# Kernel optimization log

Measured on AMD Instinct MI355X. Metric: run time of the kernel, lower is better.

Reference implementation:

```python
import jax, jax.numpy as jnp
import numpy as np

DIM = 384
HEADS = 6
HEAD_DIM = DIM // HEADS
HIDDEN = int(DIM * 4.0)
LS_INIT = 1e-5
EPS = 1e-5


def _ln(x, w, b):
    mu = jnp.mean(x, axis=-1, keepdims=True)
    var = jnp.var(x, axis=-1, keepdims=True)
    return (x - mu) * jax.lax.rsqrt(var + EPS) * w + b


def setup_inputs() -> dict:
    key = jax.random.key(0)
    ks = jax.random.split(key, 12)
    s = 0.02
    eye = jnp.eye(HIDDEN, dtype=jnp.float32)
    return {
        "x": jax.random.normal(ks[0], (8, 2048, DIM), dtype=jnp.float32),
        "qkv_w": jax.random.normal(ks[1], (3 * DIM, DIM), dtype=jnp.float32) * s,
        "qkv_b": jnp.zeros((3 * DIM,), dtype=jnp.float32),
        "proj_w": jax.random.normal(ks[2], (DIM, DIM), dtype=jnp.float32) * s,
        "proj_b": jnp.zeros((DIM,), dtype=jnp.float32),
        "fc1_w": jax.random.normal(ks[3], (HIDDEN, DIM), dtype=jnp.float32) * s,
        "fc1_b": jnp.zeros((HIDDEN,), dtype=jnp.float32),
        "eye1_w": eye + jax.random.normal(ks[4], (HIDDEN, HIDDEN), dtype=jnp.float32) * s,
        "eye2_w": eye + jax.random.normal(ks[5], (HIDDEN, HIDDEN), dtype=jnp.float32) * s,
        "fc2_w": jax.random.normal(ks[6], (DIM, HIDDEN), dtype=jnp.float32) * s,
        "fc2_b": jnp.zeros((DIM,), dtype=jnp.float32),
        "norm1_w": jnp.ones((DIM,), dtype=jnp.float32),
        "norm1_b": jnp.zeros((DIM,), dtype=jnp.float32),
        "norm2_w": jnp.ones((DIM,), dtype=jnp.float32),
        "norm2_b": jnp.zeros((DIM,), dtype=jnp.float32),
        "ls1_gamma": jnp.full((DIM,), LS_INIT, dtype=jnp.float32),
        "ls2_gamma": jnp.full((DIM,), LS_INIT, dtype=jnp.float32),
    }


def reference(x, qkv_w, qkv_b, proj_w, proj_b, fc1_w, fc1_b, eye1_w, eye2_w,
              fc2_w, fc2_b, norm1_w, norm1_b, norm2_w, norm2_b, ls1_gamma, ls2_gamma):
    B, N, C = x.shape
    scale = HEAD_DIM ** -0.5

    # ---- attention branch ----
    h = _ln(x, norm1_w, norm1_b)
    qkv = h @ qkv_w.T + qkv_b                      # [B,N,3C]
    qkv = qkv.reshape(B, N, 3, HEADS, HEAD_DIM)
    q = qkv[:, :, 0].transpose(0, 2, 1, 3) * scale  # [B,H,N,D]
    k = qkv[:, :, 1].transpose(0, 2, 1, 3)
    v = qkv[:, :, 2].transpose(0, 2, 1, 3)
    attn = jax.nn.softmax(jnp.einsum('bhnd,bhmd->bhnm', q, k), axis=-1)  # [B,H,N,N]
    o = jnp.einsum('bhnm,bhmd->bhnd', attn, v)
    o = o.transpose(0, 2, 1, 3).reshape(B, N, C)
    o = o @ proj_w.T + proj_b
    x = x + o * ls1_gamma

    # ---- extended MLP branch (timm Mlp norm is Identity) ----
    h2 = _ln(x, norm2_w, norm2_b)
    a = jax.nn.gelu(h2 @ fc1_w.T + fc1_b, approximate=False)
    a = (a @ eye1_w.T) @ eye2_w.T
    a = a @ fc2_w.T + fc2_b
    return x + a * ls2_gamma
```

## Files before the change

kernel.cpp:

```cpp
#include <hip/hip_runtime.h>
#include <math.h>

#define DIM 384
#define HEADS 6
#define HEAD_DIM 64
#define HIDDEN 1536
#define BATCH 8
#define SEQ 2048
#define TOKENS (BATCH * SEQ)

typedef __bf16 bf16;
typedef float f32x4 __attribute__((ext_vector_type(4)));
typedef float f32x16 __attribute__((ext_vector_type(16)));
typedef int i32x2 __attribute__((ext_vector_type(2)));
typedef int i32x4 __attribute__((ext_vector_type(4)));
typedef int i32x8 __attribute__((ext_vector_type(8)));

#define GLOAD_LDS(gp, lp)                                                      \
    __builtin_amdgcn_global_load_lds(                                          \
        (const __attribute__((address_space(1))) void*)(gp),                   \
        (__attribute__((address_space(3))) void*)(lp), 16, 0, 0)

__device__ __forceinline__ unsigned char to_fp8(float v) {
    return (unsigned char)(__builtin_amdgcn_cvt_pk_fp8_f32(v, v, 0, false) & 0xff);
}

__device__ __forceinline__ i32x8 pack8(i32x4 lo, i32x4 hi) {
    i32x8 r;
#pragma unroll
    for (int j = 0; j < 4; j++) { r[j] = lo[j]; r[4 + j] = hi[j]; }
    return r;
}

#define NW_QKV  (1152 * 384)
#define NW_PROJ (384 * 384)
#define NW_FC1  (1536 * 384)
#define NW_EYE  (1536 * 1536)
#define NW_FC2  (384 * 1536)
#define NW_ALL2 (NW_QKV + NW_PROJ + NW_FC1 + NW_EYE + NW_FC2)

__global__ void convert_w8(const float* __restrict__ qkv, const float* __restrict__ proj,
                           const float* __restrict__ fc1, const float* __restrict__ e2,
                           const float* __restrict__ fc2, unsigned char* __restrict__ dst) {
    int q4 = blockIdx.x * 256 + threadIdx.x;
    int stride = gridDim.x * 256;
    for (; q4 < NW_ALL2 / 4; q4 += stride) {
        int i = q4 * 4;
        int j = i;
        const float* src;
        if (j < NW_QKV) src = qkv;
        else if ((j -= NW_QKV) < NW_PROJ) src = proj;
        else if ((j -= NW_PROJ) < NW_FC1) src = fc1;
        else if ((j -= NW_FC1) < NW_EYE) src = e2;
        else { j -= NW_EYE; src = fc2; }
        float4 v = *(const float4*)(src + j);
        int p = __builtin_amdgcn_cvt_pk_fp8_f32(v.x, v.y, 0, false);
        p = __builtin_amdgcn_cvt_pk_fp8_f32(v.z, v.w, p, true);
        *(int*)(dst + i) = p;
    }
}

__global__ __launch_bounds__(256) void transpose_f8(const float* __restrict__ in,
                                                    unsigned char* __restrict__ outT) {
    __shared__ float t[64][65];
    int r0 = blockIdx.y * 64, c0 = blockIdx.x * 64;
    int tc = threadIdx.x & 63, tr = threadIdx.x >> 6;
#pragma unroll
    for (int i = 0; i < 16; i++) {
        int r = tr + 4 * i;
        t[r][tc] = in[(size_t)(r0 + r) * 1536 + c0 + tc];
    }
    __syncthreads();
    int on = threadIdx.x >> 2;
    int ok0 = (threadIdx.x & 3) * 16;
    i32x4 pk;
#pragma unroll
    for (int q = 0; q < 4; q++) {
        int p = __builtin_amdgcn_cvt_pk_fp8_f32(t[ok0 + 4 * q + 0][on],
                                                t[ok0 + 4 * q + 1][on], 0, false);
        p = __builtin_amdgcn_cvt_pk_fp8_f32(t[ok0 + 4 * q + 2][on],
                                            t[ok0 + 4 * q + 3][on], p, true);
        pk[q] = p;
    }
    *(i32x4*)(outT + (size_t)(c0 + on) * 1536 + r0 + ok0) = pk;
}

__global__ __launch_bounds__(256) void ln_kernel(const float* __restrict__ x,
                                                 const float* __restrict__ w,
                                                 const float* __restrict__ b,
                                                 unsigned char* __restrict__ out) {
    int wave = threadIdx.x >> 6;
    int lane = threadIdx.x & 63;
    int t = blockIdx.x * 4 + wave;
    const float* xr = x + (size_t)t * DIM;
    float v[6];
    float s = 0.f;
#pragma unroll
    for (int i = 0; i < 6; i++) { v[i] = xr[lane + 64 * i]; s += v[i]; }
#pragma unroll
    for (int m = 1; m < 64; m <<= 1) s += __shfl_xor(s, m, 64);
    float mu = s * (1.f / DIM);
    float q = 0.f;
#pragma unroll
    for (int i = 0; i < 6; i++) { float d = v[i] - mu; q += d * d; }
#pragma unroll
    for (int m = 1; m < 64; m <<= 1) q += __shfl_xor(q, m, 64);
    float rstd = rsqrtf(q * (1.f / DIM) + 1e-5f);
    unsigned char* orow = out + (size_t)t * DIM;
#pragma unroll
    for (int i = 0; i < 6; i++) {
        int c = lane + 64 * i;
        orow[c] = to_fp8((v[i] - mu) * rstd * w[c] + b[c]);
    }
}

template <int EPI>
__global__ __launch_bounds__(256) void gemm_f8(const unsigned char* __restrict__ A,
                                               const unsigned char* __restrict__ W,
                                               const float* __restrict__ bias,
                                               float* __restrict__ outf,
                                               const float* __restrict__ resid,
                                               const float* __restrict__ gamma,
                                               unsigned char* __restrict__ vtb8,
                                               unsigned char* __restrict__ out8,
                                               int N, int K) {
    __shared__ __attribute__((aligned(16))) unsigned char As[128 * 128];
    __shared__ __attribute__((aligned(16))) unsigned char Bs[128 * 128];
    int tid = threadIdx.x;
    int wave = tid >> 6, lane = tid & 63;
    int l15 = lane & 15, quad = lane >> 4;
    int bm = blockIdx.y * 128, bn = blockIdx.x * 128;
    int wm = (wave & 1) * 64, wn = (wave >> 1) * 64;
    f32x4 acc[4][4] = {};

    for (int k0 = 0; k0 < K; k0 += 128) {
#pragma unroll
        for (int i = 0; i < 4; i++) {
            int slot = i * 256 + tid;
            int rr = slot >> 3;
            int gg = (slot & 7) ^ (rr & 7);
            GLOAD_LDS(A + (size_t)(bm + rr) * K + k0 + gg * 16,
                      (char*)As + (i * 256 + wave * 64) * 16);
            GLOAD_LDS(W + (size_t)(bn + rr) * K + k0 + gg * 16,
                      (char*)Bs + (i * 256 + wave * 64) * 16);
        }
        __syncthreads();
        i32x8 af[4], bfr[4];
#pragma unroll
        for (int mt = 0; mt < 4; mt++) {
            int rA = wm + mt * 16 + l15;
            const i32x4* p = (const i32x4*)(As + 128 * rA);
            af[mt] = pack8(p[(2 * quad) ^ (rA & 7)], p[(2 * quad + 1) ^ (rA & 7)]);
        }
#pragma unroll
        for (int nt = 0; nt < 4; nt++) {
            int rB = wn + nt * 16 + l15;
            const i32x4* p = (const i32x4*)(Bs + 128 * rB);
            bfr[nt] = pack8(p[(2 * quad) ^ (rB & 7)], p[(2 * quad + 1) ^ (rB & 7)]);
        }
#pragma unroll
        for (int mt = 0; mt < 4; mt++)
#pragma unroll
            for (int nt = 0; nt < 4; nt++)
                acc[mt][nt] = __builtin_amdgcn_mfma_scale_f32_16x16x128_f8f6f4(
                    af[mt], bfr[nt], acc[mt][nt], 0, 0,
                    0, 0x7f7f7f7f, 0, 0x7f7f7f7f);
        __syncthreads();
    }

#pragma unroll
    for (int mt = 0; mt < 4; mt++) {
#pragma unroll
        for (int nt = 0; nt < 4; nt++) {
            int col = bn + wn + nt * 16 + l15;
            int row0 = bm + wm + mt * 16 + quad * 4;
            float v[4];
#pragma unroll
            for (int r = 0; r < 4; r++) {
                v[r] = acc[mt][nt][r];
                if (EPI >= 2) v[r] += bias[col];
                if (EPI == 2) v[r] = 0.5f * v[r] * (1.f + erff(v[r] * 0.70710678118654752f));
            }
            if (EPI == 3) {
#pragma unroll
                for (int r = 0; r < 4; r++) {
                    size_t idx = (size_t)(row0 + r) * N + col;
                    outf[idx] = resid[idx] + v[r] * gamma[col];
                }
            } else if (EPI == 4) {
                if (col < 768) {
                    float sc = (col < 384) ? 0.180336880f : 1.f;
#pragma unroll
                    for (int r = 0; r < 4; r++)
                        out8[(size_t)(row0 + r) * 768 + col] = to_fp8(v[r] * sc);
                } else {
                    int hd = col - 768;
                    int b = row0 >> 11;
                    int n0 = row0 & 2047;
                    int p = __builtin_amdgcn_cvt_pk_fp8_f32(v[0], v[1], 0, false);
                    p = __builtin_amdgcn_cvt_pk_fp8_f32(v[2], v[3], p, true);
                    *(int*)(vtb8 + ((size_t)(b * 384 + hd) << 11) + n0) = p;
                }
            } else {
#pragma unroll
                for (int r = 0; r < 4; r++)
                    out8[(size_t)(row0 + r) * N + col] = to_fp8(v[r]);
            }
        }
    }
}

__global__ __launch_bounds__(256, 3) void attn_kernel(const unsigned char* __restrict__ qk8,
                                                      const unsigned char* __restrict__ vtb8,
                                                      unsigned char* __restrict__ o) {
    __shared__ __attribute__((aligned(16))) unsigned char Ks[2][64 * 64];
    __shared__ __attribute__((aligned(16))) unsigned char Vts[2][64 * 64];
    int tid = threadIdx.x, wave = tid >> 6, lane = tid & 63;
    int l31 = lane & 31, h = lane >> 5;
    int bh = blockIdx.y;
    int b = bh / HEADS, hh = bh - b * HEADS;
    int qr0 = blockIdx.x * 128 + wave * 32;
    const unsigned char* base = qk8 + (size_t)b * SEQ * 768;
    const unsigned char* vbase = vtb8 + ((size_t)bh << 17);

    int rr = tid >> 2, ss = tid & 3;
    int fs = (rr >> 1) & 3;
    const unsigned char* kg = base + (size_t)rr * 768 + 384 + hh * 64 + 16 * (ss ^ fs);
    const unsigned char* vg = vbase + ((size_t)rr << 11) + 16 * (ss ^ fs);
    int ldsoff = tid * 16;

    i32x8 aq = *(const i32x8*)(base + (size_t)(qr0 + l31) * 768 + hh * 64 + 32 * h);

    f32x16 oa0 = {}, oa1 = {};
    float lsum = 0.f;
    int swr = (l31 >> 1) & 3;

    GLOAD_LDS(kg, (char*)Ks[0] + ldsoff);
    GLOAD_LDS(vg, (char*)Vts[0] + ldsoff);
    __syncthreads();

    for (int kt = 0; kt < SEQ / 64; kt++) {
        const unsigned char* Kc = Ks[kt & 1];
        const unsigned char* Vc = Vts[kt & 1];
        if (kt + 1 < SEQ / 64) {
            GLOAD_LDS(kg + (size_t)(kt + 1) * 64 * 768, (char*)Ks[(kt + 1) & 1] + ldsoff);
            GLOAD_LDS(vg + (kt + 1) * 64, (char*)Vts[(kt + 1) & 1] + ldsoff);
        }

        int pk[2][4];
#pragma unroll
        for (int mi = 0; mi < 2; mi++) {
            int rK = 32 * mi + l31;
            const i32x4* kp = (const i32x4*)(Kc + rK * 64);
            i32x8 ak = pack8(kp[(2 * h + 0) ^ swr], kp[(2 * h + 1) ^ swr]);
            f32x16 s = {};
            s = __builtin_amdgcn_mfma_scale_f32_32x32x64_f8f6f4(
                ak, aq, s, 0, 0, 0, 0x7f7f7f7f, 0, 0x7f7f7f7f);
#pragma unroll
            for (int g = 0; g < 4; g++) {
                float p0 = __builtin_amdgcn_exp2f(s[4 * g + 0]);
                float p1 = __builtin_amdgcn_exp2f(s[4 * g + 1]);
                float p2 = __builtin_amdgcn_exp2f(s[4 * g + 2]);
                float p3 = __builtin_amdgcn_exp2f(s[4 * g + 3]);
                lsum += (p0 + p1) + (p2 + p3);
                int pkv = __builtin_amdgcn_cvt_pk_fp8_f32(p0, p1, 0, false);
                pkv = __builtin_amdgcn_cvt_pk_fp8_f32(p2, p3, pkv, true);
                pk[mi][g] = pkv;
            }
        }

        i32x8 ap;
#pragma unroll
        for (int g = 0; g < 4; g++) {
            i32x2 r = __builtin_amdgcn_permlane32_swap(pk[0][g], pk[1][g], false, false);
            ap[2 * g] = r[0];
            ap[2 * g + 1] = r[1];
        }

        {
            const i32x4* vp0 = (const i32x4*)(Vc + l31 * 64);
            i32x8 bv0 = pack8(vp0[(2 * h + 0) ^ swr], vp0[(2 * h + 1) ^ swr]);
            oa0 = __builtin_amdgcn_mfma_scale_f32_32x32x64_f8f6f4(
                ap, bv0, oa0, 0, 0, 0, 0x7f7f7f7f, 0, 0x7f7f7f7f);
            const i32x4* vp1 = (const i32x4*)(Vc + (32 + l31) * 64);
            i32x8 bv1 = pack8(vp1[(2 * h + 0) ^ swr], vp1[(2 * h + 1) ^ swr]);
            oa1 = __builtin_amdgcn_mfma_scale_f32_32x32x64_f8f6f4(
                ap, bv1, oa1, 0, 0, 0, 0x7f7f7f7f, 0, 0x7f7f7f7f);
        }
        __syncthreads();
    }

    lsum += __shfl_xor(lsum, 32, 64);

#pragma unroll
    for (int g = 0; g < 4; g++) {
#pragma unroll
        for (int r4 = 0; r4 < 4; r4++) {
            int qloc = r4 + 8 * g + 4 * h;
            float inv = 1.f / __shfl(lsum, qloc, 64);
            int r = 4 * g + r4;
            unsigned char* orow = o + ((size_t)(b * SEQ + qr0 + qloc)) * DIM + hh * 64;
            orow[l31]      = to_fp8(oa0[r] * inv);
            orow[32 + l31] = to_fp8(oa1[r] * inv);
        }
    }
}

extern "C" void kernel_launch(void* const* d_in, const int* in_sizes, int n_in,
                              void* d_out, int out_size, void* d_ws, size_t ws_size,
                              hipStream_t stream) {
    const float* x      = (const float*)d_in[0];
    const float* qkv_w  = (const float*)d_in[1];
    const float* qkv_b  = (const float*)d_in[2];
    const float* proj_w = (const float*)d_in[3];
    const float* proj_b = (const float*)d_in[4];
    const float* fc1_w  = (const float*)d_in[5];
    const float* fc1_b  = (const float*)d_in[6];
    const float* eye1_w = (const float*)d_in[7];
    const float* eye2_w = (const float*)d_in[8];
    const float* fc2_w  = (const float*)d_in[9];
    const float* fc2_b  = (const float*)d_in[10];
    const float* n1w    = (const float*)d_in[11];
    const float* n1b    = (const float*)d_in[12];
    const float* n2w    = (const float*)d_in[13];
    const float* n2b    = (const float*)d_in[14];
    const float* ls1    = (const float*)d_in[15];
    const float* ls2    = (const float*)d_in[16];
    float* out = (float*)d_out;

    char* w = (char*)d_ws;
    size_t off = 0;
    unsigned char* w8 = (unsigned char*)(w + off); off += (size_t)NW_ALL2;
    unsigned char* wqkv8  = w8;
    unsigned char* wproj8 = wqkv8 + NW_QKV;
    unsigned char* wfc18  = wproj8 + NW_PROJ;
    unsigned char* weye28 = wfc18 + NW_FC1;
    unsigned char* wfc28  = weye28 + NW_EYE;
    unsigned char* e1t8  = (unsigned char*)(w + off); off += (size_t)NW_EYE;
    unsigned char* m1t8  = (unsigned char*)(w + off); off += (size_t)NW_EYE;
    unsigned char* wc8   = (unsigned char*)(w + off); off += (size_t)NW_FC2;
    unsigned char* hbuf8 = (unsigned char*)(w + off); off += (size_t)TOKENS * DIM;
    unsigned char* qk8   = (unsigned char*)(w + off); off += (size_t)TOKENS * 768;
    unsigned char* vtb8  = (unsigned char*)(w + off); off += (size_t)TOKENS * DIM;
    unsigned char* obuf8 = (unsigned char*)(w + off); off += (size_t)TOKENS * DIM;
    unsigned char* abuf8 = (unsigned char*)(w + off); off += (size_t)TOKENS * HIDDEN;
    float* x1   = (float*)(w + off); off += (size_t)TOKENS * DIM * 4;

    convert_w8<<<4096, 256, 0, stream>>>(qkv_w, proj_w, fc1_w, eye2_w, fc2_w, w8);

    transpose_f8<<<dim3(24, 24), 256, 0, stream>>>(eye1_w, e1t8);

    gemm_f8<0><<<dim3(1536 / 128, 1536 / 128), 256, 0, stream>>>(
        e1t8, weye28, nullptr, nullptr, nullptr, nullptr, nullptr, m1t8, 1536, 1536);

    gemm_f8<0><<<dim3(1536 / 128, 384 / 128), 256, 0, stream>>>(
        wfc28, m1t8, nullptr, nullptr, nullptr, nullptr, nullptr, wc8, 1536, 1536);

    ln_kernel<<<TOKENS / 4, 256, 0, stream>>>(x, n1w, n1b, hbuf8);

    gemm_f8<4><<<dim3(1152 / 128, TOKENS / 128), 256, 0, stream>>>(
        hbuf8, wqkv8, qkv_b, nullptr, nullptr, nullptr, vtb8, qk8, 1152, 384);

    attn_kernel<<<dim3(SEQ / 128, BATCH * HEADS), 256, 0, stream>>>(qk8, vtb8, obuf8);

    gemm_f8<3><<<dim3(384 / 128, TOKENS / 128), 256, 0, stream>>>(
        obuf8, wproj8, proj_b, x1, x, ls1, nullptr, nullptr, 384, 384);

    ln_kernel<<<TOKENS / 4, 256, 0, stream>>>(x1, n2w, n2b, hbuf8);

    gemm_f8<2><<<dim3(1536 / 128, TOKENS / 128), 256, 0, stream>>>(
        hbuf8, wfc18, fc1_b, nullptr, nullptr, nullptr, nullptr, abuf8, 1536, 384);

    gemm_f8<3><<<dim3(384 / 128, TOKENS / 128), 256, 0, stream>>>(
        abuf8, wc8, fc2_b, out, x1, ls2, nullptr, nullptr, 384, 1536);
}
```

Before: 294.9 us.

## Process 64 query rows per wave in attention to reuse K/V fragments

The attention kernel now runs 2 waves per block, and each wave handles 64 query rows as two 32-row halves instead of 32 rows. Each K and V fragment read from LDS feeds two MFMAs instead of one, halving LDS fragment reads per unit of work, and each thread issues two async global-to-LDS loads per tile instead of one. In exchange there are fewer waves per block, more accumulator registers per wave, and lower occupancy, which may reduce latency hiding.

```diff
diff --git a/kernel.cpp b/kernel.cpp
--- a/kernel.cpp
+++ b/kernel.cpp
@@ -210,98 +210,130 @@
     }
 }
 
-__global__ __launch_bounds__(256, 3) void attn_kernel(const unsigned char* __restrict__ qk8,
+__global__ __launch_bounds__(128, 2) void attn_kernel(const unsigned char* __restrict__ qk8,
                                                       const unsigned char* __restrict__ vtb8,
                                                       unsigned char* __restrict__ o) {
     __shared__ __attribute__((aligned(16))) unsigned char Ks[2][64 * 64];
     __shared__ __attribute__((aligned(16))) unsigned char Vts[2][64 * 64];
-    int tid = threadIdx.x, wave = tid >> 6, lane = tid & 63;
+    int tid = threadIdx.x, lane = tid & 63;
+    int wave = tid >> 6;
     int l31 = lane & 31, h = lane >> 5;
     int bh = blockIdx.y;
     int b = bh / HEADS, hh = bh - b * HEADS;
-    int qr0 = blockIdx.x * 128 + wave * 32;
+    int qw0 = blockIdx.x * 128 + wave * 64;
     const unsigned char* base = qk8 + (size_t)b * SEQ * 768;
     const unsigned char* vbase = vtb8 + ((size_t)bh << 17);
 
-    int rr = tid >> 2, ss = tid & 3;
-    int fs = (rr >> 1) & 3;
-    const unsigned char* kg = base + (size_t)rr * 768 + 384 + hh * 64 + 16 * (ss ^ fs);
-    const unsigned char* vg = vbase + ((size_t)rr << 11) + 16 * (ss ^ fs);
-    int ldsoff = tid * 16;
-
-    i32x8 aq = *(const i32x8*)(base + (size_t)(qr0 + l31) * 768 + hh * 64 + 32 * h);
-
-    f32x16 oa0 = {}, oa1 = {};
-    float lsum = 0.f;
+    int c0 = tid, c1 = tid + 128;
+    int rr0 = c0 >> 2, ss0 = c0 & 3, fs0 = (rr0 >> 1) & 3;
+    int rr1 = c1 >> 2, ss1 = c1 & 3, fs1 = (rr1 >> 1) & 3;
+    const unsigned char* kg0 = base + (size_t)rr0 * 768 + 384 + hh * 64 + 16 * (ss0 ^ fs0);
+    const unsigned char* kg1 = base + (size_t)rr1 * 768 + 384 + hh * 64 + 16 * (ss1 ^ fs1);
+    const unsigned char* vg0 = vbase + ((size_t)rr0 << 11) + 16 * (ss0 ^ fs0);
+    const unsigned char* vg1 = vbase + ((size_t)rr1 << 11) + 16 * (ss1 ^ fs1);
+    int lo0 = c0 * 16, lo1 = c1 * 16;
+
+    i32x8 aq0 = *(const i32x8*)(base + (size_t)(qw0 + l31) * 768 + hh * 64 + 32 * h);
+    i32x8 aq1 = *(const i32x8*)(base + (size_t)(qw0 + 32 + l31) * 768 + hh * 64 + 32 * h);
+
+    f32x16 oa00 = {}, oa01 = {}, oa10 = {}, oa11 = {};
+    float ls0 = 0.f, ls1v = 0.f;
     int swr = (l31 >> 1) & 3;
 
-    GLOAD_LDS(kg, (char*)Ks[0] + ldsoff);
-    GLOAD_LDS(vg, (char*)Vts[0] + ldsoff);
+    GLOAD_LDS(kg0, (char*)Ks[0] + lo0);
+    GLOAD_LDS(kg1, (char*)Ks[0] + lo1);
+    GLOAD_LDS(vg0, (char*)Vts[0] + lo0);
+    GLOAD_LDS(vg1, (char*)Vts[0] + lo1);
     __syncthreads();
 
     for (int kt = 0; kt < SEQ / 64; kt++) {
         const unsigned char* Kc = Ks[kt & 1];
         const unsigned char* Vc = Vts[kt & 1];
         if (kt + 1 < SEQ / 64) {
-            GLOAD_LDS(kg + (size_t)(kt + 1) * 64 * 768, (char*)Ks[(kt + 1) & 1] + ldsoff);
-            GLOAD_LDS(vg + (kt + 1) * 64, (char*)Vts[(kt + 1) & 1] + ldsoff);
-        }
-
-        int pk[2][4];
+            char* kn = (char*)Ks[(kt + 1) & 1];
+            char* vn = (char*)Vts[(kt + 1) & 1];
+            GLOAD_LDS(kg0 + (size_t)(kt + 1) * 64 * 768, kn + lo0);
+            GLOAD_LDS(kg1 + (size_t)(kt + 1) * 64 * 768, kn + lo1);
+            GLOAD_LDS(vg0 + (kt + 1) * 64, vn + lo0);
+            GLOAD_LDS(vg1 + (kt + 1) * 64, vn + lo1);
+        }
+
+        int pk[2][2][4];
 #pragma unroll
         for (int mi = 0; mi < 2; mi++) {
             int rK = 32 * mi + l31;
             const i32x4* kp = (const i32x4*)(Kc + rK * 64);
             i32x8 ak = pack8(kp[(2 * h + 0) ^ swr], kp[(2 * h + 1) ^ swr]);
-            f32x16 s = {};
-            s = __builtin_amdgcn_mfma_scale_f32_32x32x64_f8f6f4(
-                ak, aq, s, 0, 0, 0, 0x7f7f7f7f, 0, 0x7f7f7f7f);
-#pragma unroll
-            for (int g = 0; g < 4; g++) {
-                float p0 = __builtin_amdgcn_exp2f(s[4 * g + 0]);
-                float p1 = __builtin_amdgcn_exp2f(s[4 * g + 1]);
-                float p2 = __builtin_amdgcn_exp2f(s[4 * g + 2]);
-                float p3 = __builtin_amdgcn_exp2f(s[4 * g + 3]);
-                lsum += (p0 + p1) + (p2 + p3);
-                int pkv = __builtin_amdgcn_cvt_pk_fp8_f32(p0, p1, 0, false);
-                pkv = __builtin_amdgcn_cvt_pk_fp8_f32(p2, p3, pkv, true);
-                pk[mi][g] = pkv;
+#pragma unroll
+            for (int qh = 0; qh < 2; qh++) {
+                f32x16 s = {};
+                s = __builtin_amdgcn_mfma_scale_f32_32x32x64_f8f6f4(
+                    ak, (qh ? aq1 : aq0), s, 0, 0, 0, 0x7f7f7f7f, 0, 0x7f7f7f7f);
+                float lsum = 0.f;
+#pragma unroll
+                for (int g = 0; g < 4; g++) {
+                    float p0 = __builtin_amdgcn_exp2f(s[4 * g + 0]);
+                    float p1 = __builtin_amdgcn_exp2f(s[4 * g + 1]);
+                    float p2 = __builtin_amdgcn_exp2f(s[4 * g + 2]);
+                    float p3 = __builtin_amdgcn_exp2f(s[4 * g + 3]);
+                    lsum += (p0 + p1) + (p2 + p3);
+                    int pkv = __builtin_amdgcn_cvt_pk_fp8_f32(p0, p1, 0, false);
+                    pkv = __builtin_amdgcn_cvt_pk_fp8_f32(p2, p3, pkv, true);
+                    pk[qh][mi][g] = pkv;
+                }
+                if (qh) ls1v += lsum; else ls0 += lsum;
             }
         }
 
-        i32x8 ap;
+        i32x8 ap0, ap1;
 #pragma unroll
         for (int g = 0; g < 4; g++) {
-            i32x2 r = __builtin_amdgcn_permlane32_swap(pk[0][g], pk[1][g], false, false);
-            ap[2 * g] = r[0];
-            ap[2 * g + 1] = r[1];
+            i32x2 r0 = __builtin_amdgcn_permlane32_swap(pk[0][0][g], pk[0][1][g], false, false);
+            ap0[2 * g] = r0[0];
+            ap0[2 * g + 1] = r0[1];
+            i32x2 r1 = __builtin_amdgcn_permlane32_swap(pk[1][0][g], pk[1][1][g], false, false);
+            ap1[2 * g] = r1[0];
+            ap1[2 * g + 1] = r1[1];
         }
 
         {
             const i32x4* vp0 = (const i32x4*)(Vc + l31 * 64);
             i32x8 bv0 = pack8(vp0[(2 * h + 0) ^ swr], vp0[(2 * h + 1) ^ swr]);
-            oa0 = __builtin_amdgcn_mfma_scale_f32_32x32x64_f8f6f4(
-                ap, bv0, oa0, 0, 0, 0, 0x7f7f7f7f, 0, 0x7f7f7f7f);
+            oa00 = __builtin_amdgcn_mfma_scale_f32_32x32x64_f8f6f4(
+                ap0, bv0, oa00, 0, 0, 0, 0x7f7f7f7f, 0, 0x7f7f7f7f);
+            oa10 = __builtin_amdgcn_mfma_scale_f32_32x32x64_f8f6f4(
+                ap1, bv0, oa10, 0, 0, 0, 0x7f7f7f7f, 0, 0x7f7f7f7f);
             const i32x4* vp1 = (const i32x4*)(Vc + (32 + l31) * 64);
             i32x8 bv1 = pack8(vp1[(2 * h + 0) ^ swr], vp1[(2 * h + 1) ^ swr]);
-            oa1 = __builtin_amdgcn_mfma_scale_f32_32x32x64_f8f6f4(
-                ap, bv1, oa1, 0, 0, 0, 0x7f7f7f7f, 0, 0x7f7f7f7f);
+            oa01 = __builtin_amdgcn_mfma_scale_f32_32x32x64_f8f6f4(
+                ap0, bv1, oa01, 0, 0, 0, 0x7f7f7f7f, 0, 0x7f7f7f7f);
+            oa11 = __builtin_amdgcn_mfma_scale_f32_32x32x64_f8f6f4(
+                ap1, bv1, oa11, 0, 0, 0, 0x7f7f7f7f, 0, 0x7f7f7f7f);
         }
         __syncthreads();
     }
 
-    lsum += __shfl_xor(lsum, 32, 64);
+    ls0 += __shfl_xor(ls0, 32, 64);
+    ls1v += __shfl_xor(ls1v, 32, 64);
 
 #pragma unroll
     for (int g = 0; g < 4; g++) {
 #pragma unroll
         for (int r4 = 0; r4 < 4; r4++) {
             int qloc = r4 + 8 * g + 4 * h;
-            float inv = 1.f / __shfl(lsum, qloc, 64);
             int r = 4 * g + r4;
-            unsigned char* orow = o + ((size_t)(b * SEQ + qr0 + qloc)) * DIM + hh * 64;
-            orow[l31]      = to_fp8(oa0[r] * inv);
-            orow[32 + l31] = to_fp8(oa1[r] * inv);
+            {
+                float inv = 1.f / __shfl(ls0, qloc, 64);
+                unsigned char* orow = o + ((size_t)(b * SEQ + qw0 + qloc)) * DIM + hh * 64;
+                orow[l31]      = to_fp8(oa00[r] * inv);
+                orow[32 + l31] = to_fp8(oa01[r] * inv);
+            }
+            {
+                float inv = 1.f / __shfl(ls1v, qloc, 64);
+                unsigned char* orow = o + ((size_t)(b * SEQ + qw0 + 32 + qloc)) * DIM + hh * 64;
+                orow[l31]      = to_fp8(oa10[r] * inv);
+                orow[32 + l31] = to_fp8(oa11[r] * inv);
+            }
         }
     }
 }
@@ -361,7 +393,7 @@
     gemm_f8<4><<<dim3(1152 / 128, TOKENS / 128), 256, 0, stream>>>(
         hbuf8, wqkv8, qkv_b, nullptr, nullptr, nullptr, vtb8, qk8, 1152, 384);
 
-    attn_kernel<<<dim3(SEQ / 128, BATCH * HEADS), 256, 0, stream>>>(qk8, vtb8, obuf8);
+    attn_kernel<<<dim3(SEQ / 128, BATCH * HEADS), 128, 0, stream>>>(qk8, vtb8, obuf8);
 
     gemm_f8<3><<<dim3(384 / 128, TOKENS / 128), 256, 0, stream>>>(
         obuf8, wproj8, proj_b, x1, x, ls1, nullptr, nullptr, 384, 384);
```

New measurement: 304.5 us. 3.3% more time.

## Double-buffer LDS tiles in fp8 GEMM to overlap global loads with MFMA

Applied to the files above, without the earlier changes.

Doubles the shared-memory A/B tiles and prefetches the next K-tile with global_load_lds while the current tile feeds the MFMAs. This hides global-memory latency behind compute. It doubles LDS use to 64KB per block, which may lower occupancy. Correctness depends on the single barrier per iteration also covering completion of the async LDS loads.

```diff
diff --git a/kernel.cpp b/kernel.cpp
--- a/kernel.cpp
+++ b/kernel.cpp
@@ -124,8 +124,8 @@
                                                unsigned char* __restrict__ vtb8,
                                                unsigned char* __restrict__ out8,
                                                int N, int K) {
-    __shared__ __attribute__((aligned(16))) unsigned char As[128 * 128];
-    __shared__ __attribute__((aligned(16))) unsigned char Bs[128 * 128];
+    __shared__ __attribute__((aligned(16))) unsigned char As[2][128 * 128];
+    __shared__ __attribute__((aligned(16))) unsigned char Bs[2][128 * 128];
     int tid = threadIdx.x;
     int wave = tid >> 6, lane = tid & 63;
     int l15 = lane & 15, quad = lane >> 4;
@@ -133,29 +133,40 @@
     int wm = (wave & 1) * 64, wn = (wave >> 1) * 64;
     f32x4 acc[4][4] = {};
 
-    for (int k0 = 0; k0 < K; k0 += 128) {
-#pragma unroll
-        for (int i = 0; i < 4; i++) {
-            int slot = i * 256 + tid;
-            int rr = slot >> 3;
-            int gg = (slot & 7) ^ (rr & 7);
-            GLOAD_LDS(A + (size_t)(bm + rr) * K + k0 + gg * 16,
-                      (char*)As + (i * 256 + wave * 64) * 16);
-            GLOAD_LDS(W + (size_t)(bn + rr) * K + k0 + gg * 16,
-                      (char*)Bs + (i * 256 + wave * 64) * 16);
-        }
-        __syncthreads();
+    int nk = K >> 7;
+    int ldst = (tid & 192) * 16;
+#define STAGE_TILE(buf, kbase)                                                  \
+    do {                                                                        \
+        _Pragma("unroll")                                                       \
+        for (int i = 0; i < 4; i++) {                                           \
+            int slot = i * 256 + tid;                                           \
+            int rr = slot >> 3;                                                 \
+            int gg = (slot & 7) ^ (rr & 7);                                     \
+            GLOAD_LDS(A + (size_t)(bm + rr) * K + (kbase) + gg * 16,            \
+                      (char*)As[buf] + i * 4096 + ldst);                        \
+            GLOAD_LDS(W + (size_t)(bn + rr) * K + (kbase) + gg * 16,            \
+                      (char*)Bs[buf] + i * 4096 + ldst);                        \
+        }                                                                       \
+    } while (0)
+
+    STAGE_TILE(0, 0);
+    __syncthreads();
+
+    for (int kt = 0; kt < nk; kt++) {
+        int cur = kt & 1;
+        if (kt + 1 < nk) STAGE_TILE(cur ^ 1, (kt + 1) << 7);
+
         i32x8 af[4], bfr[4];
 #pragma unroll
         for (int mt = 0; mt < 4; mt++) {
             int rA = wm + mt * 16 + l15;
-            const i32x4* p = (const i32x4*)(As + 128 * rA);
+            const i32x4* p = (const i32x4*)(As[cur] + 128 * rA);
             af[mt] = pack8(p[(2 * quad) ^ (rA & 7)], p[(2 * quad + 1) ^ (rA & 7)]);
         }
 #pragma unroll
         for (int nt = 0; nt < 4; nt++) {
             int rB = wn + nt * 16 + l15;
-            const i32x4* p = (const i32x4*)(Bs + 128 * rB);
+            const i32x4* p = (const i32x4*)(Bs[cur] + 128 * rB);
             bfr[nt] = pack8(p[(2 * quad) ^ (rB & 7)], p[(2 * quad + 1) ^ (rB & 7)]);
         }
 #pragma unroll
@@ -167,6 +178,7 @@
                     0, 0x7f7f7f7f, 0, 0x7f7f7f7f);
         __syncthreads();
     }
+#undef STAGE_TILE
 
 #pragma unroll
     for (int mt = 0; mt < 4; mt++) {
```

Result: no change. 298.0 us (+1.0%).

## Fuse proj GEMM with residual and LayerNorm2; raise MFMA priority in attention

Applied to the files above, without the earlier changes.

Adds a new full-row GEMM kernel for the output projection. Each block computes 64 tokens across all 384 columns, applies bias, layer-scale and residual, writes x1, then runs LayerNorm2 in registers and writes the fp8 input for fc1. This removes the separate ln_kernel launch and its re-read of x1, at the cost of a large LDS footprint (56KB) and 96 accumulator registers per thread, which may limit occupancy. The attention kernel also wraps its MFMAs in s_setprio and hoists the second V fragment load ahead of the PV MFMAs.

```diff
diff --git a/kernel.cpp b/kernel.cpp
--- a/kernel.cpp
+++ b/kernel.cpp
@@ -210,6 +210,91 @@
     }
 }
 
+__global__ __launch_bounds__(256) void gemm_proj_ln(const unsigned char* __restrict__ A,
+                                                    const unsigned char* __restrict__ W,
+                                                    const float* __restrict__ bias,
+                                                    const float* __restrict__ resid,
+                                                    const float* __restrict__ gamma,
+                                                    const float* __restrict__ n2w,
+                                                    const float* __restrict__ n2b,
+                                                    float* __restrict__ x1,
+                                                    unsigned char* __restrict__ hbuf8) {
+    __shared__ __attribute__((aligned(16))) unsigned char As[64 * 128];
+    __shared__ __attribute__((aligned(16))) unsigned char Bs[384 * 128];
+    int tid = threadIdx.x;
+    int wave = tid >> 6, lane = tid & 63;
+    int l15 = lane & 15, quad = lane >> 4;
+    int bm = blockIdx.x * 64;
+    int wm = wave * 16;
+    f32x4 acc[24];
+#pragma unroll
+    for (int i = 0; i < 24; i++) acc[i] = (f32x4){0.f, 0.f, 0.f, 0.f};
+
+    const int K = 384;
+    for (int k0 = 0; k0 < K; k0 += 128) {
+#pragma unroll
+        for (int i = 0; i < 2; i++) {
+            int slot = i * 256 + tid;
+            int rr = slot >> 3, gg = (slot & 7) ^ (rr & 7);
+            GLOAD_LDS(A + (size_t)(bm + rr) * K + k0 + gg * 16, (char*)As + slot * 16);
+        }
+#pragma unroll
+        for (int i = 0; i < 12; i++) {
+            int slot = i * 256 + tid;
+            int rr = slot >> 3, gg = (slot & 7) ^ (rr & 7);
+            GLOAD_LDS(W + (size_t)rr * K + k0 + gg * 16, (char*)Bs + slot * 16);
+        }
+        __syncthreads();
+        int rA = wm + l15;
+        const i32x4* pa = (const i32x4*)(As + 128 * rA);
+        i32x8 af = pack8(pa[(2 * quad) ^ (rA & 7)], pa[(2 * quad + 1) ^ (rA & 7)]);
+#pragma unroll
+        for (int nt = 0; nt < 24; nt++) {
+            int rB = nt * 16 + l15;
+            const i32x4* pb = (const i32x4*)(Bs + 128 * rB);
+            i32x8 bf = pack8(pb[(2 * quad) ^ (rB & 7)], pb[(2 * quad + 1) ^ (rB & 7)]);
+            acc[nt] = __builtin_amdgcn_mfma_scale_f32_16x16x128_f8f6f4(
+                af, bf, acc[nt], 0, 0, 0, 0x7f7f7f7f, 0, 0x7f7f7f7f);
+        }
+        __syncthreads();
+    }
+
+    int row0 = bm + wm + quad * 4;
+#pragma unroll
+    for (int nt = 0; nt < 24; nt++) {
+        int col = nt * 16 + l15;
+        float bi = bias[col], ga = gamma[col];
+#pragma unroll
+        for (int r = 0; r < 4; r++) {
+            size_t idx = (size_t)(row0 + r) * DIM + col;
+            float v = resid[idx] + (acc[nt][r] + bi) * ga;
+            x1[idx] = v;
+            acc[nt][r] = v;
+        }
+    }
+#pragma unroll
+    for (int r = 0; r < 4; r++) {
+        float s = 0.f;
+#pragma unroll
+        for (int nt = 0; nt < 24; nt++) s += acc[nt][r];
+#pragma unroll
+        for (int m = 1; m < 16; m <<= 1) s += __shfl_xor(s, m, 64);
+        float mu = s * (1.f / DIM);
+        float q = 0.f;
+#pragma unroll
+        for (int nt = 0; nt < 24; nt++) { float d = acc[nt][r] - mu; q += d * d; }
+#pragma unroll
+        for (int m = 1; m < 16; m <<= 1) q += __shfl_xor(q, m, 64);
+        float rstd = rsqrtf(q * (1.f / DIM) + 1e-5f);
+        unsigned char* orow = hbuf8 + (size_t)(row0 + r) * DIM;
+#pragma unroll
+        for (int nt = 0; nt < 24; nt++) {
+            int col = nt * 16 + l15;
+            orow[col] = to_fp8((acc[nt][r] - mu) * rstd * n2w[col] + n2b[col]);
+        }
+    }
+}
+
 __global__ __launch_bounds__(256, 3) void attn_kernel(const unsigned char* __restrict__ qk8,
                                                       const unsigned char* __restrict__ vtb8,
                                                       unsigned char* __restrict__ o) {
@@ -254,8 +339,10 @@
             const i32x4* kp = (const i32x4*)(Kc + rK * 64);
             i32x8 ak = pack8(kp[(2 * h + 0) ^ swr], kp[(2 * h + 1) ^ swr]);
             f32x16 s = {};
+            __builtin_amdgcn_s_setprio(1);
             s = __builtin_amdgcn_mfma_scale_f32_32x32x64_f8f6f4(
                 ak, aq, s, 0, 0, 0, 0x7f7f7f7f, 0, 0x7f7f7f7f);
+            __builtin_amdgcn_s_setprio(0);
 #pragma unroll
             for (int g = 0; g < 4; g++) {
                 float p0 = __builtin_amdgcn_exp2f(s[4 * g + 0]);
@@ -280,12 +367,14 @@
         {
             const i32x4* vp0 = (const i32x4*)(Vc + l31 * 64);
             i32x8 bv0 = pack8(vp0[(2 * h + 0) ^ swr], vp0[(2 * h + 1) ^ swr]);
+            const i32x4* vp1 = (const i32x4*)(Vc + (32 + l31) * 64);
+            i32x8 bv1 = pack8(vp1[(2 * h + 0) ^ swr], vp1[(2 * h + 1) ^ swr]);
+            __builtin_amdgcn_s_setprio(1);
             oa0 = __builtin_amdgcn_mfma_scale_f32_32x32x64_f8f6f4(
                 ap, bv0, oa0, 0, 0, 0, 0x7f7f7f7f, 0, 0x7f7f7f7f);
-            const i32x4* vp1 = (const i32x4*)(Vc + (32 + l31) * 64);
-            i32x8 bv1 = pack8(vp1[(2 * h + 0) ^ swr], vp1[(2 * h + 1) ^ swr]);
             oa1 = __builtin_amdgcn_mfma_scale_f32_32x32x64_f8f6f4(
                 ap, bv1, oa1, 0, 0, 0, 0x7f7f7f7f, 0, 0x7f7f7f7f);
+            __builtin_amdgcn_s_setprio(0);
         }
         __syncthreads();
     }
@@ -363,10 +452,8 @@
 
     attn_kernel<<<dim3(SEQ / 128, BATCH * HEADS), 256, 0, stream>>>(qk8, vtb8, obuf8);
 
-    gemm_f8<3><<<dim3(384 / 128, TOKENS / 128), 256, 0, stream>>>(
-        obuf8, wproj8, proj_b, x1, x, ls1, nullptr, nullptr, 384, 384);
-
-    ln_kernel<<<TOKENS / 4, 256, 0, stream>>>(x1, n2w, n2b, hbuf8);
+    gemm_proj_ln<<<TOKENS / 64, 256, 0, stream>>>(
+        obuf8, wproj8, proj_b, x, ls1, n2w, n2b, x1, hbuf8);
 
     gemm_f8<2><<<dim3(1536 / 128, TOKENS / 128), 256, 0, stream>>>(
         hbuf8, wfc18, fc1_b, nullptr, nullptr, nullptr, nullptr, abuf8, 1536, 384);
```

Result: no change. 298.3 us (+1.2%).
